# Kernel optimization log

Hardware: AMD Instinct MI355X
Metric: run time of the kernel (lower is better)

## Reference

```python
import jax, jax.numpy as jnp
import numpy as np
from jax.scipy.linalg import expm

D_LOGIC = 128
D_MEM = 16
SO_DIM = D_MEM * (D_MEM - 1) // 2  # 120


def _linear_init(key, fan_in, shape):
    bound = 1.0 / np.sqrt(fan_in)
    return jax.random.uniform(key, shape, jnp.float32, -bound, bound)


def setup_inputs() -> dict:
    key = jax.random.key(0)
    ks = jax.random.split(key, 14)
    B, S = 4, 128
    return {
        "x_logic": jax.random.normal(ks[0], (B, S, D_LOGIC), jnp.float32),
        "x_memory": jax.random.normal(ks[1], (B, S, D_MEM), jnp.float32),
        # W_Q / W_K
        "Wq": _linear_init(ks[2], D_LOGIC, (D_LOGIC, D_LOGIC)),
        "bq": _linear_init(ks[3], D_LOGIC, (D_LOGIC,)),
        "Wk": _linear_init(ks[4], D_LOGIC, (D_LOGIC, D_LOGIC)),
        "bk": _linear_init(ks[5], D_LOGIC, (D_LOGIC,)),
        # gamma_net: Linear(d_logic, 2*d_logic) -> Tanh -> Linear(2*d_logic, so_dim)
        "W1": _linear_init(ks[6], D_LOGIC, (2 * D_LOGIC, D_LOGIC)),
        "b1": _linear_init(ks[7], D_LOGIC, (2 * D_LOGIC,)),
        "W2": _linear_init(ks[8], 2 * D_LOGIC, (SO_DIM, 2 * D_LOGIC)),
        "b2": _linear_init(ks[9], 2 * D_LOGIC, (SO_DIM,)),
        # out_proj: Linear(d_memory, d_memory)
        "Wo": _linear_init(ks[10], D_MEM, (D_MEM, D_MEM)),
        "bo": _linear_init(ks[11], D_MEM, (D_MEM,)),
    }


def reference(x_logic, x_memory, Wq, bq, Wk, bk, W1, b1, W2, b2, Wo, bo):
    B, S, d_logic = x_logic.shape
    dm = x_memory.shape[-1]

    # attention over logic stream
    Q = x_logic @ Wq.T + bq
    K = x_logic @ Wk.T + bk
    attn = jax.nn.softmax(
        jnp.einsum("bjd,bid->bji", Q, K) / jnp.sqrt(jnp.float32(d_logic)), axis=-1
    )  # [B, S(j), S(i)]

    # per-pair Lie-algebra params: delta[b,j,i] = x_logic[b,j] - x_logic[b,i]
    delta = x_logic[:, :, None, :] - x_logic[:, None, :, :]  # [B,S,S,d_logic]
    h = jnp.tanh(delta @ W1.T + b1)
    lie = h @ W2.T + b2  # [B,S,S,so_dim]

    # scatter into skew-symmetric matrices [B,S,S,dm,dm]
    r, c = np.triu_indices(dm, k=1)
    skew = jnp.zeros((B, S, S, dm, dm), x_logic.dtype)
    skew = skew.at[..., r, c].set(lie)
    skew = skew.at[..., c, r].set(-lie)

    # Lie-group exponential -> orthogonal transport matrices
    T_all = expm(skew)  # [B,S,S,dm,dm]

    # transported[b,j,i,:] = T[b,j,i] @ x_memory[b,i]
    transported = jnp.einsum("bjide,bie->bjid", T_all, x_memory)

    # attention-weighted aggregation over i
    settled = jnp.einsum("bji,bjid->bjd", attn, transported)  # [B,S,dm]

    out = settled @ Wo.T + bo
    return out, T_all
```

## Files before the change

### kernel.cpp

```cpp
#include <hip/hip_runtime.h>
#include <hip/hip_fp16.h>

#define S_LEN 128
#define DLOG  128
#define DMEM  16
#define SO    120
#define HDIM  256

typedef _Float16 v8h __attribute__((ext_vector_type(8)));
typedef __fp16 v2hf __attribute__((ext_vector_type(2)));
typedef float v4f __attribute__((ext_vector_type(4)));

union PkU { v2hf h; unsigned u; };
union V8U { v8h v; int u[4]; };

__device__ __forceinline__ v8h splat8(float x) {
  _Float16 h = (_Float16)x;
  v8h v = {h, h, h, h, h, h, h, h};
  return v;
}

__global__ __launch_bounds__(512) void qku_kernel(
    const float* __restrict__ xl, const float* __restrict__ Wq,
    const float* __restrict__ bq, const float* __restrict__ Wk,
    const float* __restrict__ bk, const float* __restrict__ W1,
    float* __restrict__ Q, float* __restrict__ K, float* __restrict__ u) {
  int bj = blockIdx.x, t = threadIdx.x;
  int lane = t & 63, wu = t >> 6;
  int half = lane >> 5, l5 = lane & 31;
  float4 xv = *(const float4*)(xl + bj * 128 + 4 * l5);
  int seg = wu >> 1;
  const float* wb;
  if (seg == 0) wb = Wq;
  else if (seg == 1) wb = Wk - 128 * 128;
  else wb = W1 - 256 * 128;
  #pragma unroll 4
  for (int step = 0; step < 32; ++step) {
    int ro = wu * 64 + 2 * step + half;
    float4 wv = *(const float4*)(wb + ro * 128 + 4 * l5);
    float v = fmaf(wv.x, xv.x, fmaf(wv.y, xv.y, fmaf(wv.z, xv.z, wv.w * xv.w)));
    v += __shfl_xor(v, 1, 64);
    v += __shfl_xor(v, 2, 64);
    v += __shfl_xor(v, 4, 64);
    v += __shfl_xor(v, 8, 64);
    v += __shfl_xor(v, 16, 64);
    if (l5 == 0) {
      if (seg == 0) Q[bj * 128 + ro] = v + bq[ro];
      else if (seg == 1) K[bj * 128 + (ro - 128)] = v + bk[ro - 128];
      else u[bj * 256 + (ro - 256)] = v;
    }
  }
}

__global__ __launch_bounds__(256) void attn_kernel(
    const float* __restrict__ Q, const float* __restrict__ K,
    float* __restrict__ attn) {
  int t = threadIdx.x;
  int sub = t >> 7, t128 = t & 127;
  int bj = blockIdx.x * 2 + sub, b = bj >> 7;
  int lane = t & 63, wu = (t >> 6) & 1;
  int half = lane >> 5, l5 = lane & 31;
  __shared__ float sc[2][128];
  __shared__ float red[2][128];
  float4 qv = *(const float4*)(Q + bj * 128 + 4 * l5);
  #pragma unroll 4
  for (int step = 0; step < 32; ++step) {
    int ro = wu * 64 + 2 * step + half;
    float4 kv = *(const float4*)(K + (size_t)(b * 128 + ro) * 128 + 4 * l5);
    float v = fmaf(kv.x, qv.x, fmaf(kv.y, qv.y, fmaf(kv.z, qv.z, kv.w * qv.w)));
    v += __shfl_xor(v, 1, 64);
    v += __shfl_xor(v, 2, 64);
    v += __shfl_xor(v, 4, 64);
    v += __shfl_xor(v, 8, 64);
    v += __shfl_xor(v, 16, 64);
    if (l5 == 0) sc[sub][ro] = v * 0.08838834764831845f;
  }
  __syncthreads();
  int i = t128;
  float s = sc[sub][i];
  red[sub][i] = s;
  __syncthreads();
  for (int off = 64; off; off >>= 1) {
    if (i < off) red[sub][i] = fmaxf(red[sub][i], red[sub][i + off]);
    __syncthreads();
  }
  float m = red[sub][0];
  __syncthreads();
  float e = expf(s - m);
  red[sub][i] = e;
  __syncthreads();
  for (int off = 64; off; off >>= 1) {
    if (i < off) red[sub][i] += red[sub][i + off];
    __syncthreads();
  }
  attn[(size_t)bj * 128 + i] = e / red[sub][0];
}

__global__ __launch_bounds__(512) void lie_kernel(
    const float* __restrict__ W2g, const float* __restrict__ b2g,
    const float* __restrict__ ug, const float* __restrict__ b1g,
    float* __restrict__ Tg) {
  __shared__ _Float16 w2t[128 * 136];
  __shared__ float ujb[256];
  int t = threadIdx.x, lane = t & 63;
  int wu = __builtin_amdgcn_readfirstlane(t >> 6);
  int bj = blockIdx.x;
  int b = bj >> 7;
  int nn = lane & 15, q = lane >> 4;
  int irow = wu * 16 + nn;

  if (t < 256) ujb[t] = ug[bj * 256 + t] + b1g[t];
  for (int idx = t; idx < 1088; idx += 512) w2t[16320 + idx] = (_Float16)0.f;

  v4f acc[8];
  #pragma unroll
  for (int tt = 0; tt < 8; ++tt) acc[tt] = (v4f){0.f, 0.f, 0.f, 0.f};

  const float* uib = ug + (size_t)(b * 128 + irow) * 256;

  for (int khalf = 0; khalf < 2; ++khalf) {
    __syncthreads();
    for (int idx = t; idx < 3840; idx += 512) {
      int row = idx >> 5, c4 = (idx & 31) * 4;
      float4 v = *(const float4*)(W2g + row * 256 + khalf * 128 + c4);
      PkU a, b2;
      a.h = __builtin_amdgcn_cvt_pkrtz(v.x, v.y);
      b2.h = __builtin_amdgcn_cvt_pkrtz(v.z, v.w);
      uint2 pk = {a.u, b2.u};
      *(uint2*)(w2t + row * 136 + c4) = pk;
    }
    __syncthreads();
    #pragma unroll
    for (int ks = 0; ks < 4; ++ks) {
      int k0 = khalf * 128 + ks * 32 + 8 * q;
      float4 ui0 = *(const float4*)(uib + k0);
      float4 ui1 = *(const float4*)(uib + k0 + 4);
      float4 uj0 = *(const float4*)(ujb + k0);
      float4 uj1 = *(const float4*)(ujb + k0 + 4);
      float xv[8] = {uj0.x - ui0.x, uj0.y - ui0.y, uj0.z - ui0.z,
                     uj0.w - ui0.w, uj1.x - ui1.x, uj1.y - ui1.y,
                     uj1.z - ui1.z, uj1.w - ui1.w};
      float rv[8];
      #pragma unroll
      for (int k = 0; k < 8; ++k) {
        float x = xv[k];
        float ax = fabsf(x);
        float e = __expf(-2.f * ax);
        float r = __fdividef(1.f - e, 1.f + e);
        rv[k] = copysignf(r, x);
      }
      V8U ah;
      #pragma unroll
      for (int k = 0; k < 4; ++k) {
        PkU pu;
        pu.h = __builtin_amdgcn_cvt_pkrtz(rv[2 * k], rv[2 * k + 1]);
        ah.u[k] = (int)pu.u;
      }
      #pragma unroll
      for (int tt = 0; tt < 8; ++tt) {
        const v8h bf = *(const v8h*)(w2t + (16 * tt + nn) * 136 + ks * 32 + 8 * q);
        acc[tt] = __builtin_amdgcn_mfma_f32_16x16x32_f16(ah.v, bf, acc[tt], 0, 0, 0);
      }
    }
  }

  int rc0[8], rc1[8];
  float bbv[8];
  bool val[8];
  #pragma unroll
  for (int tt = 0; tt < 8; ++tt) {
    int n16 = 16 * tt + nn;
    val[tt] = (n16 < 120);
    float fr_ = floorf((31.0f - sqrtf(961.0f - 8.0f * (float)n16)) * 0.5f);
    int r = (int)fr_;
    int Sr = 15 * r - ((r * (r - 1)) >> 1);
    int c = n16 - Sr + r + 1;
    rc0[tt] = r * 16 + c;
    rc1[tt] = c * 16 + r;
    bbv[tt] = val[tt] ? b2g[n16] : 0.f;
  }

  _Float16* hw = (_Float16*)Tg;
  _Float16* aSt = w2t;
  for (int pass = 0; pass < 2; ++pass) {
    __syncthreads();
    #pragma unroll
    for (int reg = 0; reg < 4; ++reg) {
      int pidx = 4 * q + reg;
      if ((pidx >> 3) == pass) {
        _Float16* ab = aSt + (wu * 8 + (pidx & 7)) * 256;
        #pragma unroll
        for (int tt = 0; tt < 8; ++tt) {
          if (val[tt]) {
            _Float16 hv = (_Float16)(acc[tt][reg] + bbv[tt]);
            ab[rc0[tt]] = hv;
            ab[rc1[tt]] = -hv;
          }
        }
        ab[nn * 17] = (_Float16)0.f;
      }
    }
    __syncthreads();
    #pragma unroll
    for (int k = 0; k < 4; ++k) {
      int unit = t + k * 512;
      int lp = unit >> 5, off = (unit & 31) * 8;
      int g = bj * 128 + (lp >> 3) * 16 + pass * 8 + (lp & 7);
      *(v8h*)(hw + (size_t)g * 512 + 256 + off) = *(const v8h*)(aSt + lp * 256 + off);
    }
  }
}

__device__ __forceinline__ void split8(const float* x, v8h& hi, v8h& lo) {
  union U { v8h v; v2hf p[4]; } H, L;
  #pragma unroll
  for (int i = 0; i < 4; ++i) {
    float a = x[2 * i], b = x[2 * i + 1];
    v2hf h = __builtin_amdgcn_cvt_pkrtz(a, b);
    float ra = (float)h[0], rb = (float)h[1];
    v2hf l = __builtin_amdgcn_cvt_pkrtz(a - ra, b - rb);
    H.p[i] = h;
    L.p[i] = l;
  }
  hi = H.v;
  lo = L.v;
}

__global__ __launch_bounds__(256) void expm_kernel(
    float* __restrict__ Tg, const float* __restrict__ attn,
    const float* __restrict__ xm, float* __restrict__ part) {
  __shared__ float ErB_all[4][1280];
  __shared__ float sred[4][16];
  int t = threadIdx.x, lane = t & 63;
  int wu = __builtin_amdgcn_readfirstlane(t >> 6);
  int pbase = blockIdx.x * 16 + wu * 4;
  int nn = lane & 15, q = lane >> 4, b8 = (q & 1) * 8;
  float* ErW = ErB_all[wu];
  const _Float16* hf = (const _Float16*)Tg;

  int idxA = ((2 * (q & 1)) * 16 + nn) * 4;
  int idxB = idxA + 64;

  float scv[4];
  int sv[4];
  V8U Apk[4];
  v4f Af[4];
  #pragma unroll
  for (int j = 0; j < 4; ++j) {
    size_t p = (size_t)(pbase + j);
    const _Float16* Ap = hf + p * 512 + 256;
    v8h rowh = *(const v8h*)(Ap + nn * 16 + b8);
    float s2 = 0.f;
    #pragma unroll
    for (int k = 0; k < 8; ++k) {
      float xf = (float)rowh[k];
      s2 = fmaf(xf, xf, s2);
    }
    #pragma unroll
    for (int off = 1; off < 64; off <<= 1) s2 += __shfl_xor(s2, off, 64);
    float bound = 0.5f * sqrtf(s2);
    int bb = __float_as_int(bound);
    int s = ((bb >> 23) & 255) - 126;
    s = min(max(s, 0), 12);
    sv[j] = __builtin_amdgcn_readfirstlane(s);
    scv[j] = __int_as_float((127 - sv[j]) << 23);
    v8h sch = splat8(scv[j]);
    V8U ap;
    ap.v = rowh * sch;
    #pragma unroll
    for (int i = 0; i < 4; ++i) Apk[j].u[i] = ap.u[i];
    #pragma unroll
    for (int reg = 0; reg < 4; ++reg)
      Af[j][reg] = (float)Ap[(4 * q + reg) * 16 + nn] * scv[j];
  }

  V8U IC1, IC2;
  #pragma unroll
  for (int i = 0; i < 4; ++i) {
    float d0 = (b8 + 2 * i == nn) ? 1.f : 0.f;
    float d1 = (b8 + 2 * i + 1 == nn) ? 1.f : 0.f;
    PkU u1, u2;
    u1.h = __builtin_amdgcn_cvt_pkrtz(10.666667f * d0, 10.666667f * d1);
    u2.h = __builtin_amdgcn_cvt_pkrtz(2.1333333f * d0, 2.1333333f * d1);
    IC1.u[i] = (int)u1.u;
    IC2.u[i] = (int)u2.u;
  }
  v8h k1a = splat8(7.9365079e-4f);
  v8h k1b = splat8(0.17777778f);
  v8h k2a = splat8(8.8183422e-5f);
  v8h k2b = splat8(2.5396825e-2f);
  v4f z4 = {0.f, 0.f, 0.f, 0.f};

  v4f cB[4];
  #pragma unroll
  for (int j = 0; j < 4; ++j) {
    V8U bfa;
    #pragma unroll
    for (int i = 0; i < 4; ++i) bfa.u[i] = Apk[j].u[i] ^ 0x80008000;
    cB[j] = __builtin_amdgcn_mfma_f32_16x16x32_f16(Apk[j].v, bfa.v, z4, 0, 0, 0);
  }

  V8U fB[4];
  #pragma unroll
  for (int j = 0; j < 4; ++j) {
    PkU u0, u1;
    u0.h = __builtin_amdgcn_cvt_pkrtz(cB[j][0], cB[j][1]);
    u1.h = __builtin_amdgcn_cvt_pkrtz(cB[j][2], cB[j][3]);
    fB[j].u[0] = __builtin_amdgcn_ds_bpermute(idxA, (int)u0.u);
    fB[j].u[1] = __builtin_amdgcn_ds_bpermute(idxA, (int)u1.u);
    fB[j].u[2] = __builtin_amdgcn_ds_bpermute(idxB, (int)u0.u);
    fB[j].u[3] = __builtin_amdgcn_ds_bpermute(idxB, (int)u1.u);
  }

  V8U fB2[4];
  #pragma unroll
  for (int j = 0; j < 4; ++j) {
    v4f c = __builtin_amdgcn_mfma_f32_16x16x32_f16(fB[j].v, fB[j].v, z4, 0, 0, 0);
    PkU u0, u1;
    u0.h = __builtin_amdgcn_cvt_pkrtz(c[0], c[1]);
    u1.h = __builtin_amdgcn_cvt_pkrtz(c[2], c[3]);
    fB2[j].u[0] = __builtin_amdgcn_ds_bpermute(idxA, (int)u0.u);
    fB2[j].u[1] = __builtin_amdgcn_ds_bpermute(idxA, (int)u1.u);
    fB2[j].u[2] = __builtin_amdgcn_ds_bpermute(idxB, (int)u0.u);
    fB2[j].u[3] = __builtin_amdgcn_ds_bpermute(idxB, (int)u1.u);
  }

  v4f E[4];
  #pragma unroll
  for (int j = 0; j < 4; ++j) {
    V8U M1, M2;
    M1.v = fB2[j].v * k1a + (fB[j].v * k1b + IC1.v);
    M2.v = fB2[j].v * k2a + (fB[j].v * k2b + IC2.v);
    v4f c3m = __builtin_amdgcn_mfma_f32_16x16x32_f16(M1.v, fB2[j].v, z4, 0, 0, 0);
    v4f c4m = __builtin_amdgcn_mfma_f32_16x16x32_f16(M2.v, fB2[j].v, z4, 0, 0, 0);
    v4f Cc, Qc;
    #pragma unroll
    for (int reg = 0; reg < 4; ++reg) {
      float dg = (4 * q + reg == nn) ? 1.f : 0.f;
      Cc[reg] = fmaf(c3m[reg], 2.44140625e-4f,
                     fmaf(cB[j][reg], 0.25f, dg + Af[j][reg]));
      Qc[reg] = fmaf(c4m[reg], 2.44140625e-4f, cB[j][reg] * 0.083333333f);
    }
    PkU u0, u1;
    u0.h = __builtin_amdgcn_cvt_pkrtz(Qc[0], Qc[1]);
    u1.h = __builtin_amdgcn_cvt_pkrtz(Qc[2], Qc[3]);
    V8U fQ;
    fQ.u[0] = __builtin_amdgcn_ds_bpermute(idxA, (int)u0.u);
    fQ.u[1] = __builtin_amdgcn_ds_bpermute(idxA, (int)u1.u);
    fQ.u[2] = __builtin_amdgcn_ds_bpermute(idxB, (int)u0.u);
    fQ.u[3] = __builtin_amdgcn_ds_bpermute(idxB, (int)u1.u);
    v4f c5 = __builtin_amdgcn_mfma_f32_16x16x32_f16(Apk[j].v, fQ.v, z4, 0, 0, 0);
    E[j] = Cc + c5 * 0.5f;
  }

  int smax = max(max(sv[0], sv[1]), max(sv[2], sv[3]));
  for (int it = 0; it < smax; ++it) {
    #pragma unroll
    for (int j = 0; j < 4; ++j) {
      if (it < sv[j]) {
        float* Erp = ErW + j * 320;
        PkU u0, u1;
        u0.h = __builtin_amdgcn_cvt_pkrtz(E[j][0], E[j][1]);
        u1.h = __builtin_amdgcn_cvt_pkrtz(E[j][2], E[j][3]);
        V8U bfe;
        bfe.u[0] = __builtin_amdgcn_ds_bpermute(idxA, (int)u0.u);
        bfe.u[1] = __builtin_amdgcn_ds_bpermute(idxA, (int)u1.u);
        bfe.u[2] = __builtin_amdgcn_ds_bpermute(idxB, (int)u0.u);
        bfe.u[3] = __builtin_amdgcn_ds_bpermute(idxB, (int)u1.u);
        #pragma unroll
        for (int reg = 0; reg < 4; ++reg)
          Erp[(4 * q + reg) * 20 + nn] = E[j][reg];
        asm volatile("s_waitcnt lgkmcnt(0)" ::: "memory");
        float4 a0 = *(const float4*)(Erp + nn * 20 + b8);
        float4 a1 = *(const float4*)(Erp + nn * 20 + b8 + 4);
        float xa[8] = {a0.x, a0.y, a0.z, a0.w, a1.x, a1.y, a1.z, a1.w};
        v8h ahi, alo;
        split8(xa, ahi, alo);
        v8h Ecat = (q < 2) ? ahi : alo;
        v4f z = {0.f, 0.f, 0.f, 0.f};
        E[j] = __builtin_amdgcn_mfma_f32_16x16x32_f16(Ecat, bfe.v, z, 0, 0, 0);
      }
    }
  }

  float pacc[4] = {0.f, 0.f, 0.f, 0.f};
  #pragma unroll
  for (int j = 0; j < 4; ++j) {
    int p = pbase + j;
    float* dst = Tg + (size_t)p * 256;
    #pragma unroll
    for (int reg = 0; reg < 4; ++reg)
      dst[(4 * q + reg) * 16 + nn] = E[j][reg];
    int b = p >> 14, i = p & 127;
    float xv = xm[((b << 7) + i) * 16 + nn];
    float aw = attn[(size_t)p] * xv;
    #pragma unroll
    for (int reg = 0; reg < 4; ++reg)
      pacc[reg] = fmaf(aw, E[j][reg], pacc[reg]);
  }
  #pragma unroll
  for (int reg = 0; reg < 4; ++reg) {
    #pragma unroll
    for (int off = 1; off < 16; off <<= 1)
      pacc[reg] += __shfl_xor(pacc[reg], off, 64);
  }
  if (nn == 0) {
    #pragma unroll
    for (int reg = 0; reg < 4; ++reg) sred[wu][4 * q + reg] = pacc[reg];
  }
  __syncthreads();
  if (t < 16)
    part[(size_t)blockIdx.x * 16 + t] =
        sred[0][t] + sred[1][t] + sred[2][t] + sred[3][t];
}

__global__ __launch_bounds__(64) void settle_fin_kernel(
    const float* __restrict__ part, const float* __restrict__ Wo,
    const float* __restrict__ bo, float* __restrict__ outp) {
  int bj = blockIdx.x, t = threadIdx.x;
  int r = t & 15, e0 = t >> 4;
  const float* pb = part + (size_t)bj * 128;
  float s = pb[e0 * 16 + r] + pb[(e0 + 4) * 16 + r];
  __shared__ float sf[64];
  sf[t] = s;
  __syncthreads();
  if (t < 16) sf[t] = sf[t] + sf[16 + t] + sf[32 + t] + sf[48 + t];
  __syncthreads();
  if (t < 16) {
    float o = bo[t];
    const float* wr = Wo + t * 16;
    #pragma unroll
    for (int c = 0; c < 16; ++c) o = fmaf(wr[c], sf[c], o);
    outp[bj * 16 + t] = o;
  }
}

extern "C" void kernel_launch(void* const* d_in, const int* in_sizes, int n_in,
                              void* d_out, int out_size, void* d_ws,
                              size_t ws_size, hipStream_t stream) {
  const float* xl = (const float*)d_in[0];
  const float* xm = (const float*)d_in[1];
  const float* Wq = (const float*)d_in[2];
  const float* bq = (const float*)d_in[3];
  const float* Wk = (const float*)d_in[4];
  const float* bk = (const float*)d_in[5];
  const float* W1 = (const float*)d_in[6];
  const float* b1 = (const float*)d_in[7];
  const float* W2 = (const float*)d_in[8];
  const float* b2 = (const float*)d_in[9];
  const float* Wo = (const float*)d_in[10];
  const float* bo = (const float*)d_in[11];
  float* outp = (float*)d_out;
  float* Tg = outp + 8192;
  float* wsf = (float*)d_ws;
  float* Q = wsf;
  float* K = wsf + 65536;
  float* attn = wsf + 131072;
  float* u = wsf + 196608;
  float* part = wsf + 196608;

  hipLaunchKernelGGL(qku_kernel, dim3(512), dim3(512), 0, stream, xl, Wq, bq, Wk, bk, W1, Q, K, u);
  hipLaunchKernelGGL(attn_kernel, dim3(256), dim3(256), 0, stream, Q, K, attn);
  hipLaunchKernelGGL(lie_kernel, dim3(512), dim3(512), 0, stream, W2, b2, u, b1, Tg);
  hipLaunchKernelGGL(expm_kernel, dim3(4096), dim3(256), 0, stream, Tg, attn, xm, part);
  hipLaunchKernelGGL(settle_fin_kernel, dim3(512), dim3(64), 0, stream, part, Wo, bo, outp);
}
```

Baseline: 190.1 us.

## Precast W2 to fp16 once and derive expm scaling from A^2 norm

```diff
diff --git a/kernel.cpp b/kernel.cpp
--- a/kernel.cpp
+++ b/kernel.cpp
@@ -24,8 +24,20 @@
     const float* __restrict__ xl, const float* __restrict__ Wq,
     const float* __restrict__ bq, const float* __restrict__ Wk,
     const float* __restrict__ bk, const float* __restrict__ W1,
-    float* __restrict__ Q, float* __restrict__ K, float* __restrict__ u) {
+    const float* __restrict__ W2g, float* __restrict__ Q,
+    float* __restrict__ K, float* __restrict__ u, float* __restrict__ Tg) {
   int bj = blockIdx.x, t = threadIdx.x;
+  if (bj >= 512) {
+    int idx = (bj - 512) * 2048 + t * 4;
+    float4 v = *(const float4*)(W2g + idx);
+    PkU a, b;
+    a.h = __builtin_amdgcn_cvt_pkrtz(v.x, v.y);
+    b.h = __builtin_amdgcn_cvt_pkrtz(v.z, v.w);
+    uint2 pk = {a.u, b.u};
+    _Float16* w2hT = (_Float16*)Tg;
+    *(uint2*)(w2hT + (idx >> 8) * 512 + (idx & 255)) = pk;
+    return;
+  }
   int lane = t & 63, wu = t >> 6;
   int half = lane >> 5, l5 = lane & 31;
   float4 xv = *(const float4*)(xl + bj * 128 + 4 * l5);
@@ -97,9 +109,8 @@
 }
 
 __global__ __launch_bounds__(512) void lie_kernel(
-    const float* __restrict__ W2g, const float* __restrict__ b2g,
-    const float* __restrict__ ug, const float* __restrict__ b1g,
-    float* __restrict__ Tg) {
+    const float* __restrict__ b2g, const float* __restrict__ ug,
+    const float* __restrict__ b1g, float* __restrict__ Tg) {
   __shared__ _Float16 w2t[128 * 136];
   __shared__ float ujb[256];
   int t = threadIdx.x, lane = t & 63;
@@ -108,6 +119,7 @@
   int b = bj >> 7;
   int nn = lane & 15, q = lane >> 4;
   int irow = wu * 16 + nn;
+  const _Float16* w2hT = (const _Float16*)Tg;
 
   if (t < 256) ujb[t] = ug[bj * 256 + t] + b1g[t];
   for (int idx = t; idx < 1088; idx += 512) w2t[16320 + idx] = (_Float16)0.f;
@@ -120,14 +132,10 @@
 
   for (int khalf = 0; khalf < 2; ++khalf) {
     __syncthreads();
-    for (int idx = t; idx < 3840; idx += 512) {
-      int row = idx >> 5, c4 = (idx & 31) * 4;
-      float4 v = *(const float4*)(W2g + row * 256 + khalf * 128 + c4);
-      PkU a, b2;
-      a.h = __builtin_amdgcn_cvt_pkrtz(v.x, v.y);
-      b2.h = __builtin_amdgcn_cvt_pkrtz(v.z, v.w);
-      uint2 pk = {a.u, b2.u};
-      *(uint2*)(w2t + row * 136 + c4) = pk;
+    for (int idx = t; idx < 1920; idx += 512) {
+      int row = idx >> 4, cu = (idx & 15) * 8;
+      *(v8h*)(w2t + row * 136 + cu) =
+          *(const v8h*)(w2hT + row * 512 + khalf * 128 + cu);
     }
     __syncthreads();
     #pragma unroll
@@ -241,8 +249,6 @@
   int idxA = ((2 * (q & 1)) * 16 + nn) * 4;
   int idxB = idxA + 64;
 
-  float scv[4];
-  int sv[4];
   V8U Apk[4];
   v4f Af[4];
   #pragma unroll
@@ -250,28 +256,46 @@
     size_t p = (size_t)(pbase + j);
     const _Float16* Ap = hf + p * 512 + 256;
     v8h rowh = *(const v8h*)(Ap + nn * 16 + b8);
-    float s2 = 0.f;
-    #pragma unroll
-    for (int k = 0; k < 8; ++k) {
-      float xf = (float)rowh[k];
-      s2 = fmaf(xf, xf, s2);
-    }
-    #pragma unroll
-    for (int off = 1; off < 64; off <<= 1) s2 += __shfl_xor(s2, off, 64);
-    float bound = 0.5f * sqrtf(s2);
-    int bb = __float_as_int(bound);
-    int s = ((bb >> 23) & 255) - 126;
-    s = min(max(s, 0), 12);
+    V8U ap;
+    ap.v = rowh;
+    #pragma unroll
+    for (int i = 0; i < 4; ++i) Apk[j].u[i] = ap.u[i];
+    #pragma unroll
+    for (int reg = 0; reg < 4; ++reg)
+      Af[j][reg] = (float)Ap[(4 * q + reg) * 16 + nn];
+  }
+
+  v4f z4 = {0.f, 0.f, 0.f, 0.f};
+
+  v4f cB[4];
+  #pragma unroll
+  for (int j = 0; j < 4; ++j) {
+    V8U bfa;
+    #pragma unroll
+    for (int i = 0; i < 4; ++i) bfa.u[i] = Apk[j].u[i] ^ 0x80008000;
+    cB[j] = __builtin_amdgcn_mfma_f32_16x16x32_f16(Apk[j].v, bfa.v, z4, 0, 0, 0);
+  }
+
+  int sv[4];
+  #pragma unroll
+  for (int j = 0; j < 4; ++j) {
+    float cs = fabsf(cB[j][0]) + fabsf(cB[j][1]) + fabsf(cB[j][2]) +
+               fabsf(cB[j][3]);
+    cs += __shfl_xor(cs, 16, 64);
+    cs += __shfl_xor(cs, 32, 64);
+    cs = fmaxf(cs, __shfl_xor(cs, 1, 64));
+    cs = fmaxf(cs, __shfl_xor(cs, 2, 64));
+    cs = fmaxf(cs, __shfl_xor(cs, 4, 64));
+    cs = fmaxf(cs, __shfl_xor(cs, 8, 64));
+    float x = cs * 0.5f;
+    int e = ((__float_as_int(x) >> 23) & 255) - 127;
+    int s = min(12, max(0, (e + 2) >> 1));
     sv[j] = __builtin_amdgcn_readfirstlane(s);
-    scv[j] = __int_as_float((127 - sv[j]) << 23);
-    v8h sch = splat8(scv[j]);
-    V8U ap;
-    ap.v = rowh * sch;
-    #pragma unroll
-    for (int i = 0; i < 4; ++i) Apk[j].u[i] = ap.u[i];
-    #pragma unroll
-    for (int reg = 0; reg < 4; ++reg)
-      Af[j][reg] = (float)Ap[(4 * q + reg) * 16 + nn] * scv[j];
+    float sc = __int_as_float((127 - sv[j]) << 23);
+    float sc2 = sc * sc;
+    cB[j] = cB[j] * sc2;
+    Apk[j].v = Apk[j].v * splat8(sc);
+    Af[j] = Af[j] * sc;
   }
 
   V8U IC1, IC2;
@@ -289,16 +313,6 @@
   v8h k1b = splat8(0.17777778f);
   v8h k2a = splat8(8.8183422e-5f);
   v8h k2b = splat8(2.5396825e-2f);
-  v4f z4 = {0.f, 0.f, 0.f, 0.f};
-
-  v4f cB[4];
-  #pragma unroll
-  for (int j = 0; j < 4; ++j) {
-    V8U bfa;
-    #pragma unroll
-    for (int i = 0; i < 4; ++i) bfa.u[i] = Apk[j].u[i] ^ 0x80008000;
-    cB[j] = __builtin_amdgcn_mfma_f32_16x16x32_f16(Apk[j].v, bfa.v, z4, 0, 0, 0);
-  }
 
   V8U fB[4];
   #pragma unroll
@@ -459,9 +473,9 @@
   float* u = wsf + 196608;
   float* part = wsf + 196608;
 
-  hipLaunchKernelGGL(qku_kernel, dim3(512), dim3(512), 0, stream, xl, Wq, bq, Wk, bk, W1, Q, K, u);
+  hipLaunchKernelGGL(qku_kernel, dim3(527), dim3(512), 0, stream, xl, Wq, bq, Wk, bk, W1, W2, Q, K, u, Tg);
   hipLaunchKernelGGL(attn_kernel, dim3(256), dim3(256), 0, stream, Q, K, attn);
-  hipLaunchKernelGGL(lie_kernel, dim3(512), dim3(512), 0, stream, W2, b2, u, b1, Tg);
+  hipLaunchKernelGGL(lie_kernel, dim3(512), dim3(512), 0, stream, b2, u, b1, Tg);
   hipLaunchKernelGGL(expm_kernel, dim3(4096), dim3(256), 0, stream, Tg, attn, xm, part);
   hipLaunchKernelGGL(settle_fin_kernel, dim3(512), dim3(64), 0, stream, part, Wo, bo, outp);
 }
```

Result: no change. 187.6 us (-1.3%).
